# Kernel tuning notes

Hardware: AMD Instinct MI355X
Metric: run time of the kernel (lower is better)

The kernel has to match this reference:

```python
import math
import jax, jax.numpy as jnp
import numpy as np

B, C, T = 8, 512, 8192
UP, DOWN, UP_K, DOWN_K = 2, 2, 12, 12


def kaiser_sinc_filter1d(cutoff, half_width, kernel_size):
    even = kernel_size % 2 == 0
    half_size = kernel_size // 2
    delta_f = 4 * half_width
    A = 2.285 * (half_size - 1) * math.pi * delta_f + 7.95
    if A > 50.0:
        beta = 0.1102 * (A - 8.7)
    elif A >= 21.0:
        beta = 0.5842 * (A - 21) ** 0.4 + 0.07886 * (A - 21.0)
    else:
        beta = 0.0
    window = np.kaiser(kernel_size, beta)
    if even:
        time = np.arange(-half_size, half_size) + 0.5
    else:
        time = np.arange(kernel_size) - half_size
    filt = 2 * cutoff * window * np.sinc(2 * cutoff * time)
    filt = filt / filt.sum()
    return jnp.asarray(filt, dtype=jnp.float32)


def setup_inputs() -> dict:
    key = jax.random.key(0)
    k1, k2, k3 = jax.random.split(key, 3)
    x = jax.random.normal(k1, (B, C, T), dtype=jnp.float32)
    alpha = 0.1 * jax.random.normal(k2, (1, C, 1), dtype=jnp.float32)
    beta = 0.1 * jax.random.normal(k3, (1, C, 1), dtype=jnp.float32)
    up_filter = kaiser_sinc_filter1d(0.5 / UP, 0.6 / UP, UP_K)      # [UP_K]
    down_filter = kaiser_sinc_filter1d(0.5 / DOWN, 0.6 / DOWN, DOWN_K)  # [DOWN_K]
    return {"x": x, "alpha": alpha, "beta": beta,
            "up_filter": up_filter, "down_filter": down_filter}


def _depthwise_kernel(filt, channels):
    # [k] -> [C, 1, k] depthwise kernel (OIH layout)
    return jnp.broadcast_to(filt[None, None, :], (channels, 1, filt.shape[0]))


def _upsample(x, filt, ratio, k):
    # replicate pad, depthwise conv_transpose (via lhs dilation), trim edges
    c = x.shape[1]
    pad = k // ratio - 1
    pad_left = pad * ratio + (k - ratio) // 2
    pad_right = pad * ratio + (k - ratio + 1) // 2
    xp = jnp.pad(x, ((0, 0), (0, 0), (pad, pad)), mode='edge')
    # conv_transpose == conv with flipped kernel, input dilated by stride,
    # full padding (k-1) on each side
    w = _depthwise_kernel(filt[::-1], c)
    y = ratio * jax.lax.conv_general_dilated(
        xp, w, window_strides=(1,), padding=[(k - 1, k - 1)],
        lhs_dilation=(ratio,), feature_group_count=c,
        dimension_numbers=('NCH', 'OIH', 'NCH'))
    return y[..., pad_left:-pad_right]  # [B, C, T*ratio]


def _downsample(x, filt, ratio, k):
    # replicate-pad low-pass depthwise conv with stride=ratio
    c = x.shape[1]
    even = k % 2 == 0
    pad_left = k // 2 - int(even)
    pad_right = k // 2
    xp = jnp.pad(x, ((0, 0), (0, 0), (pad_left, pad_right)), mode='edge')
    w = _depthwise_kernel(filt, c)
    return jax.lax.conv_general_dilated(
        xp, w, window_strides=(ratio,), padding='VALID',
        feature_group_count=c, dimension_numbers=('NCH', 'OIH', 'NCH'))


def _snake_beta(x, alpha, beta):
    a = jnp.exp(alpha)
    b = jnp.exp(beta)
    s = jnp.sin(x * a)
    return x + (s * s) / (b + 1e-9)


def reference(x, alpha, beta, up_filter, down_filter):
    y = _upsample(x, up_filter, UP, UP_K)        # [B, C, T*UP]
    y = _snake_beta(y, alpha, beta)
    y = _downsample(y, down_filter, DOWN, DOWN_K)  # [B, C, T]
    return y
```

## Files before the change

kernel.cpp:

```cpp
#include <hip/hip_runtime.h>
#include <hip/hip_bf16.h>

namespace {
constexpr int T_LEN = 8192;
constexpr int C_CH  = 512;
constexpr int B_SZ  = 8;
constexpr int TILE  = 2048;
constexpr int NTH   = 256;
constexpr int TPR   = T_LEN / TILE;
constexpr int NS    = TILE + 6;
constexpr int XSZ   = TILE + 12;
constexpr int ZSZ   = 2 * TILE + 12;
}

__global__ __launch_bounds__(NTH)
void aaa_fused(const float* __restrict__ x,
               const float* __restrict__ alpha,
               const float* __restrict__ beta,
               const float* __restrict__ upf,
               const float* __restrict__ dnf,
               float* __restrict__ out)
{
    __shared__ float xs[XSZ];
    __shared__ float zs[ZSZ];

    const int tid  = threadIdx.x;
    const int bid  = blockIdx.x;
    const int tile = bid & (TPR - 1);
    const int row  = bid / TPR;
    const int ch   = row & (C_CH - 1);
    const int n0   = tile * TILE;

    const float* __restrict__ xr = x + (size_t)row * T_LEN;
    float* __restrict__ outr     = out + (size_t)row * T_LEN;

    const float av = expf(alpha[ch]);
    const float rb = 1.0f / (expf(beta[ch]) + 1e-9f);

    float cE[6], cO[6], fd[12];
#pragma unroll
    for (int i = 0; i < 6; ++i) {
        cE[i] = 2.0f * upf[11 - 2 * i];
        cO[i] = 2.0f * upf[10 - 2 * i];
    }
#pragma unroll
    for (int i = 0; i < 12; ++i) fd[i] = dnf[i];

    for (int i = tid; i < XSZ; i += NTH) {
        int g = n0 - 6 + i;
        g = min(max(g, 0), T_LEN - 1);
        xs[i] = xr[g];
    }
    __syncthreads();

    for (int si = tid; si < NS; si += NTH) {
        const float x0 = xs[si + 0];
        const float x1 = xs[si + 1];
        const float x2 = xs[si + 2];
        const float x3 = xs[si + 3];
        const float x4 = xs[si + 4];
        const float x5 = xs[si + 5];
        const float x6 = xs[si + 6];
        float ye = cE[0]*x0 + cE[1]*x1 + cE[2]*x2 + cE[3]*x3 + cE[4]*x4 + cE[5]*x5;
        float yo = cO[0]*x1 + cO[1]*x2 + cO[2]*x3 + cO[3]*x4 + cO[4]*x5 + cO[5]*x6;
        const float se = sinf(ye * av);
        const float so = sinf(yo * av);
        zs[2 * si + 0] = ye + se * se * rb;
        zs[2 * si + 1] = yo + so * so * rb;
    }
    __syncthreads();

#pragma unroll
    for (int k = 0; k < TILE / NTH; ++k) {
        const int ln = tid + k * NTH;
        const int n  = n0 + ln;
        float acc = 0.0f;
        if (n >= 3 && n <= T_LEN - 4) {
            const int base = 2 * ln + 1;
#pragma unroll
            for (int j = 0; j < 12; ++j) acc += fd[j] * zs[base + j];
        } else {
            const int m0 = 2 * n0 - 6;
#pragma unroll
            for (int j = 0; j < 12; ++j) {
                int m = 2 * n - 5 + j;
                m = min(max(m, 0), 2 * T_LEN - 1);
                acc += fd[j] * zs[m - m0];
            }
        }
        outr[n] = acc;
    }
}

extern "C" void kernel_launch(void* const* d_in, const int* in_sizes, int n_in,
                              void* d_out, int out_size, void* d_ws, size_t ws_size,
                              hipStream_t stream)
{
    (void)in_sizes; (void)n_in; (void)out_size; (void)d_ws; (void)ws_size;
    const float* x     = (const float*)d_in[0];
    const float* alpha = (const float*)d_in[1];
    const float* beta  = (const float*)d_in[2];
    const float* upf   = (const float*)d_in[3];
    const float* dnf   = (const float*)d_in[4];
    float* out = (float*)d_out;

    dim3 grid(B_SZ * C_CH * TPR);
    dim3 block(NTH);
    aaa_fused<<<grid, block, 0, stream>>>(x, alpha, beta, upf, dnf, out);
}
```

Before: 287.4 us.

## Use cosine identity for snake, vectorize loads and downsample with packed float2

```diff
diff --git a/kernel.cpp b/kernel.cpp
--- a/kernel.cpp
+++ b/kernel.cpp
@@ -1,5 +1,7 @@
 #include <hip/hip_runtime.h>
 #include <hip/hip_bf16.h>
+
+typedef float v2f __attribute__((ext_vector_type(2)));
 
 namespace {
 constexpr int T_LEN = 8192;
@@ -9,7 +11,8 @@
 constexpr int NTH   = 256;
 constexpr int TPR   = T_LEN / TILE;
 constexpr int NS    = TILE + 6;
-constexpr int XSZ   = TILE + 12;
+constexpr int XOFF  = 8;
+constexpr int XSZ   = XOFF + TILE + 8;
 constexpr int ZSZ   = 2 * TILE + 12;
 }
 
@@ -21,8 +24,8 @@
                const float* __restrict__ dnf,
                float* __restrict__ out)
 {
-    __shared__ float xs[XSZ];
-    __shared__ float zs[ZSZ];
+    __shared__ __align__(16) float xs[XSZ];
+    __shared__ __align__(16) float zs[ZSZ];
 
     const int tid  = threadIdx.x;
     const int bid  = blockIdx.x;
@@ -34,61 +37,79 @@
     const float* __restrict__ xr = x + (size_t)row * T_LEN;
     float* __restrict__ outr     = out + (size_t)row * T_LEN;
 
-    const float av = expf(alpha[ch]);
-    const float rb = 1.0f / (expf(beta[ch]) + 1e-9f);
+    const float av  = expf(alpha[ch]);
+    const float rb  = 1.0f / (expf(beta[ch]) + 1e-9f);
+    const float avp = av * 0.3183098861837907f;
+    const float hrb = 0.5f * rb;
 
-    float cE[6], cO[6], fd[12];
+    float cE[6], cO[6];
 #pragma unroll
     for (int i = 0; i < 6; ++i) {
         cE[i] = 2.0f * upf[11 - 2 * i];
         cO[i] = 2.0f * upf[10 - 2 * i];
     }
+    v2f w[7];
+    w[0] = v2f{0.0f, dnf[0]};
 #pragma unroll
-    for (int i = 0; i < 12; ++i) fd[i] = dnf[i];
+    for (int k = 1; k < 6; ++k) w[k] = v2f{dnf[2 * k - 1], dnf[2 * k]};
+    w[6] = v2f{dnf[11], 0.0f};
 
-    for (int i = tid; i < XSZ; i += NTH) {
-        int g = n0 - 6 + i;
-        g = min(max(g, 0), T_LEN - 1);
-        xs[i] = xr[g];
+    {
+        const float4* __restrict__ xr4 = reinterpret_cast<const float4*>(xr + n0);
+        float4* xs4 = reinterpret_cast<float4*>(xs + XOFF);
+        xs4[tid]       = xr4[tid];
+        xs4[tid + NTH] = xr4[tid + NTH];
+        if (tid < 6) {
+            int gl = max(n0 - 6 + tid, 0);
+            xs[XOFF - 6 + tid] = xr[gl];
+            int gr = min(n0 + TILE + tid, T_LEN - 1);
+            xs[XOFF + TILE + tid] = xr[gr];
+        }
     }
     __syncthreads();
 
     for (int si = tid; si < NS; si += NTH) {
-        const float x0 = xs[si + 0];
-        const float x1 = xs[si + 1];
-        const float x2 = xs[si + 2];
-        const float x3 = xs[si + 3];
-        const float x4 = xs[si + 4];
-        const float x5 = xs[si + 5];
-        const float x6 = xs[si + 6];
+        const float x0 = xs[si + 2];
+        const float x1 = xs[si + 3];
+        const float x2 = xs[si + 4];
+        const float x3 = xs[si + 5];
+        const float x4 = xs[si + 6];
+        const float x5 = xs[si + 7];
+        const float x6 = xs[si + 8];
         float ye = cE[0]*x0 + cE[1]*x1 + cE[2]*x2 + cE[3]*x3 + cE[4]*x4 + cE[5]*x5;
         float yo = cO[0]*x1 + cO[1]*x2 + cO[2]*x3 + cO[3]*x4 + cO[4]*x5 + cO[5]*x6;
-        const float se = sinf(ye * av);
-        const float so = sinf(yo * av);
-        zs[2 * si + 0] = ye + se * se * rb;
-        zs[2 * si + 1] = yo + so * so * rb;
+        float ue = ye * avp;  ue -= floorf(ue);
+        float uo = yo * avp;  uo -= floorf(uo);
+        const float ce = __builtin_amdgcn_cosf(ue);
+        const float co = __builtin_amdgcn_cosf(uo);
+        const float z0 = (ye + hrb) - hrb * ce;
+        const float z1 = (yo + hrb) - hrb * co;
+        reinterpret_cast<v2f*>(zs)[si] = v2f{z0, z1};
     }
     __syncthreads();
 
+    const v2f* __restrict__ zs2 = reinterpret_cast<const v2f*>(zs);
 #pragma unroll
     for (int k = 0; k < TILE / NTH; ++k) {
         const int ln = tid + k * NTH;
         const int n  = n0 + ln;
-        float acc = 0.0f;
         if (n >= 3 && n <= T_LEN - 4) {
-            const int base = 2 * ln + 1;
+            v2f acc = w[0] * zs2[ln];
 #pragma unroll
-            for (int j = 0; j < 12; ++j) acc += fd[j] * zs[base + j];
+            for (int j = 1; j < 7; ++j) acc += w[j] * zs2[ln + j];
+            outr[n] = acc.x + acc.y;
         } else {
             const int m0 = 2 * n0 - 6;
+            float acc = 0.0f;
 #pragma unroll
             for (int j = 0; j < 12; ++j) {
                 int m = 2 * n - 5 + j;
                 m = min(max(m, 0), 2 * T_LEN - 1);
-                acc += fd[j] * zs[m - m0];
+                const float fj = (j & 1) ? w[(j + 1) >> 1].x : w[j >> 1].y;
+                acc += fj * zs[m - m0];
             }
+            outr[n] = acc;
         }
-        outr[n] = acc;
     }
 }
 
```

Result: faster. 234.0 us (-18.6%).
